# Optimization experiments

Hardware: AMD Instinct MI355X
Metric: run time of the kernel (lower is better)

## Reference

```python
import math
import jax, jax.numpy as jnp
import numpy as np
from jax import lax

N, C, H, W = 16, 128, 56, 56


def _conv(x, w, padding, dilation=(1, 1), groups=1):
    # NCHW conv matching torch.nn.Conv2d semantics (bias=False)
    return lax.conv_general_dilated(
        x, w, window_strides=(1, 1),
        padding=[(padding[0], padding[0]), (padding[1], padding[1])],
        rhs_dilation=dilation,
        dimension_numbers=('NCHW', 'OIHW', 'NCHW'),
        feature_group_count=groups)


def setup_inputs() -> dict:
    key = jax.random.key(0)
    ks = jax.random.split(key, 6)
    x = jax.random.normal(ks[0], (N, C, H, W), jnp.float32)
    w2 = jax.random.normal(ks[1], (C, C, 1, 3), jnp.float32) * 0.05   # dense 1x3 conv
    p6w = jax.random.normal(ks[2], (1, C, 7, 1), jnp.float32) * 0.02  # trunc_normal std=0.02
    w7 = jax.random.normal(ks[3], (C, 1, 1, 5), jnp.float32) * 0.05   # depthwise 1x5
    w8 = jax.random.normal(ks[4], (C, 1, 5, 5), jnp.float32) * 0.05   # depthwise 5x5 dil=2
    p9w = jax.random.normal(ks[5], (1, 1, 7, C), jnp.float32) * 0.02
    return {"x": x, "w2": w2, "p6w": p6w, "w7": w7, "w8": w8, "p9w": p9w}


def reference(x, w2, p6w, w7, w8, p9w):
    n, c, h, w = x.shape
    # t_1: F.unfold(x, (1,7), dilation=(1,2), padding=(0,6)) -> (n, c, 7, h, w)
    # tap k reads column j + 2k - 6 of x (zero padded)
    xp = jnp.pad(x, ((0, 0), (0, 0), (0, 0), (6, 6)))
    t1 = jnp.stack([xp[..., 2 * k:2 * k + w] for k in range(7)], axis=2)
    # t_2: dense (1,3) conv, padding (0,1)
    t2 = _conv(x, w2, (0, 1))
    # t_3: windowed channel correlation, (n, c, 7, c)
    t3 = jnp.einsum('nakhw,nbhw->nakb', t1, x) / math.sqrt(h * w)
    # t_4: F.unfold(t_2, (7,1), padding=(3,0)) -> (n, c, 7, h, w), taps along height
    t2p = jnp.pad(t2, ((0, 0), (0, 0), (3, 3), (0, 0)))
    t4 = jnp.stack([t2p[:, :, k:k + h, :] for k in range(7)], axis=2)
    # elementwise weighting
    t6 = p6w * t3          # (1,c,7,1) broadcast over (n,c,7,c)
    # depthwise convs
    t7 = _conv(t2, w7, (0, 2), groups=c)                 # (1,5) depthwise
    t8 = _conv(x, w8, (4, 4), dilation=(2, 2), groups=c)  # (5,5) depthwise, dil 2
    t9 = p9w * t6          # (1,1,7,c) broadcast
    # t_10: contract (c_in, tap) against windowed t4 -> (n, c, h, w)
    t10 = jnp.einsum('nakb,nakhw->nbhw', t9, t4) / math.sqrt(c * 7)
    t11 = t10 - t7
    t12 = t8 - t11
    return t12
```

## Files before the change

### kernel.cpp

```cpp
#include <hip/hip_runtime.h>

#define N_ 16
#define C_ 128
#define H_ 56
#define W_ 56
#define HW_ 3136

typedef __bf16 bf16x8 __attribute__((ext_vector_type(8)));
typedef __bf16 bf16x2 __attribute__((ext_vector_type(2)));
typedef float f32x4 __attribute__((ext_vector_type(4)));

#define XT_PER_N 401408
#define T2_PLANE 3472
#define T2_PER_N 444416
#define S_PER_N 114688
#define T10_PER_N 401408

#define WS_T10_OFF   3670016u
#define WS_T3_OFF    12845056u
#define WS_T2PB_OFF  20185088u
#define WS_W2B_OFF   34406400u

__global__ __launch_bounds__(256) void f0_prep(const float* __restrict__ x,
                                               const float* __restrict__ w2,
                                               __bf16* __restrict__ xT,
                                               __bf16* __restrict__ w2b,
                                               __bf16* __restrict__ t2pb) {
    int bid = blockIdx.x;
    int tid = threadIdx.x;
    if (bid < 2048) {
        int c = bid & 127, n = bid >> 7;
        __shared__ float xs[56 * 57];
        const float* xp = x + (size_t)(n * C_ + c) * HW_;
        for (int i = tid; i < HW_; i += 256) {
            int h = i / 56, w = i - 56 * h;
            xs[w * 57 + h] = xp[i];
        }
        __syncthreads();
        __bf16* op = xT + (size_t)(n * C_ + c) * HW_;
        for (int i = tid; i < 1568; i += 256) {
            int j = 2 * i;
            int wp = j / 56, h = j - 56 * wp;
            bf16x2 pr = {(__bf16)xs[wp * 57 + h], (__bf16)xs[wp * 57 + h + 1]};
            *(bf16x2*)&op[j] = pr;
        }
        __bf16* tp = t2pb + (size_t)(n * C_ + c) * T2_PLANE;
        for (int i = tid; i < 336; i += 256)
            tp[(i < 168) ? i : (3136 + i)] = (__bf16)0.f;
    } else {
        int idx = (bid - 2048) * 256 + tid;
        int co = idx / 384, kk = idx - co * 384;
        int j = kk >> 7, ci = kk & 127;
        w2b[idx] = (__bf16)w2[co * 384 + ci * 3 + j];
    }
}

__global__ __launch_bounds__(256) void f1_main(const float* __restrict__ x,
                                               const __bf16* __restrict__ w2b,
                                               const __bf16* __restrict__ xT,
                                               __bf16* __restrict__ t2pb,
                                               float* __restrict__ t3) {
    __shared__ __align__(16) char smem[36864];
    int bid = blockIdx.x;
    int tid = threadIdx.x;
    int wv = tid >> 6, lane = tid & 63;
    int lm = lane & 15, lq = lane >> 4;
    int wi = wv >> 1, wj = wv & 1;

    if (bid < 448) {
        int hc = bid & 3;
        int k = (bid >> 2) % 7;
        int n = bid / 28;
        int w_lo = 6 - 2 * k; if (w_lo < 0) w_lo = 0;
        int w_hi = 62 - 2 * k; if (w_hi > 56) w_hi = 56;
        int jlo = w_lo * 56;
        int L = (w_hi - w_lo) * 56;
        int T = (L + 63) >> 6;
        int shiftA = (2 * k - 6) * 56;

        __bf16* As = (__bf16*)smem;
        __bf16* Bs = (__bf16*)(smem + 18432);

        f32x4 acc[4][4];
        f32x4 zero4 = {0.f, 0.f, 0.f, 0.f};
#pragma unroll
        for (int i = 0; i < 4; i++)
#pragma unroll
            for (int j = 0; j < 4; j++) acc[i][j] = zero4;

        const __bf16* Ag = xT + (size_t)n * XT_PER_N + jlo + shiftA;
        const __bf16* Bg = xT + (size_t)n * XT_PER_N + jlo;
        __bf16 bz = (__bf16)0.f;
        bf16x8 vzero = {bz, bz, bz, bz, bz, bz, bz, bz};

        for (int c = hc; c < T; c += 4) {
            int off0 = c * 64;
#pragma unroll
            for (int u = 0; u < 4; u++) {
                int v = tid + u * 256;
                int m = v & 7, a = v >> 3;
                int jo = off0 + 8 * m;
                bool val = (jo + 8 <= L);
                bf16x8 va = val ? *(const bf16x8*)(Ag + (size_t)a * HW_ + jo) : vzero;
                bf16x8 vb = val ? *(const bf16x8*)(Bg + (size_t)a * HW_ + jo) : vzero;
                *(bf16x8*)&As[a * 72 + 8 * m] = va;
                *(bf16x8*)&Bs[a * 72 + 8 * m] = vb;
            }
            __syncthreads();
#pragma unroll
            for (int kb = 0; kb < 2; kb++) {
                bf16x8 av[4], bv[4];
#pragma unroll
                for (int i = 0; i < 4; i++)
                    av[i] = *(const bf16x8*)&As[(wi * 64 + i * 16 + lm) * 72 + kb * 32 + lq * 8];
#pragma unroll
                for (int j = 0; j < 4; j++)
                    bv[j] = *(const bf16x8*)&Bs[(wj * 64 + j * 16 + lm) * 72 + kb * 32 + lq * 8];
#pragma unroll
                for (int i = 0; i < 4; i++)
#pragma unroll
                    for (int j = 0; j < 4; j++)
                        acc[i][j] = __builtin_amdgcn_mfma_f32_16x16x32_bf16(av[i], bv[j], acc[i][j], 0, 0, 0);
            }
            __syncthreads();
        }

        float* t3p = t3 + (size_t)(n * 7 + k) * (C_ * C_);
        const float inv56 = 1.0f / 56.0f;
#pragma unroll
        for (int i = 0; i < 4; i++)
#pragma unroll
            for (int j = 0; j < 4; j++)
#pragma unroll
                for (int r = 0; r < 4; r++) {
                    int a = wi * 64 + i * 16 + lq * 4 + r;
                    int b = wj * 64 + j * 16 + lm;
                    atomicAdd(&t3p[a * C_ + b], acc[i][j][r] * inv56);
                }
    } else {
        int idx = bid - 448;
        int h = idx % 56, n = idx / 56;
        __bf16* Bs = (__bf16*)smem;
        float* kbuf = (float*)(smem + 17952);

        const float* xn = x + (size_t)n * C_ * HW_ + h * 56;
        for (int i = tid; i < 66 * 128; i += 256) {
            int ci = i / 66, wp = i - 66 * ci;
            int wx = wp - 1;
            float v = (wx >= 0 && wx < 56) ? xn[ci * HW_ + wx] : 0.f;
            Bs[wp * 136 + ci] = (__bf16)v;
        }

        f32x4 acc[4][2];
        f32x4 zero4 = {0.f, 0.f, 0.f, 0.f};
#pragma unroll
        for (int i = 0; i < 4; i++)
#pragma unroll
            for (int j = 0; j < 2; j++) acc[i][j] = zero4;

        __bf16* Asc = (__bf16*)(smem + 17952);
        __syncthreads();

        for (int c6 = 0; c6 < 6; c6++) {
#pragma unroll
            for (int u = 0; u < 4; u++) {
                int v = tid + u * 256;
                int m = v & 7, co = v >> 3;
                *(bf16x8*)&Asc[co * 72 + 8 * m] =
                    *(const bf16x8*)(w2b + co * 384 + c6 * 64 + 8 * m);
            }
            __syncthreads();
#pragma unroll
            for (int kl = 0; kl < 2; kl++) {
                int ks = c6 * 2 + kl;
                int j = ks >> 2;
                int cbase = (ks & 3) * 32;
                bf16x8 av[4], bv[2];
#pragma unroll
                for (int i = 0; i < 4; i++)
                    av[i] = *(const bf16x8*)&Asc[(wi * 64 + i * 16 + lm) * 72 + kl * 32 + lq * 8];
#pragma unroll
                for (int jt = 0; jt < 2; jt++) {
                    int row = wj * 32 + jt * 16 + lm + j;
                    bv[jt] = *(const bf16x8*)&Bs[row * 136 + cbase + lq * 8];
                }
#pragma unroll
                for (int i = 0; i < 4; i++)
#pragma unroll
                    for (int jt = 0; jt < 2; jt++)
                        acc[i][jt] = __builtin_amdgcn_mfma_f32_16x16x32_bf16(av[i], bv[jt], acc[i][jt], 0, 0, 0);
            }
            __syncthreads();
        }

        __bf16* t2n = t2pb + (size_t)n * T2_PER_N;
#pragma unroll 1
        for (int i = 0; i < 4; i++) {
            __syncthreads();
#pragma unroll
            for (int jt = 0; jt < 2; jt++)
#pragma unroll
                for (int r = 0; r < 4; r++)
                    kbuf[(wi * 16 + lq * 4 + r) * 65 + wj * 32 + jt * 16 + lm] = acc[i][jt][r];
            __syncthreads();
            int row = tid >> 3, seg = tid & 7;
            if (seg < 7) {
                int co = (row < 16) ? (i * 16 + row) : (64 + i * 16 + (row - 16));
                const float* src = &kbuf[row * 65 + seg * 8];
                bf16x8 o8;
#pragma unroll
                for (int d = 0; d < 8; d++) o8[d] = (__bf16)src[d];
                *(bf16x8*)(t2n + (size_t)co * T2_PLANE + (h + 3) * 56 + seg * 8) = o8;
            }
        }
    }
}

__global__ __launch_bounds__(256) void sprep(const float* __restrict__ t3,
                                             const float* __restrict__ p6w,
                                             const float* __restrict__ p9w,
                                             __bf16* __restrict__ s) {
    int idx = blockIdx.x * 256 + threadIdx.x;
    int n = idx / S_PER_N;
    int rem = idx - n * S_PER_N;
    int b = rem / 896;
    int ak = rem - b * 896;
    int a = ak / 7, k = ak - 7 * a;
    const float rs = 0.03340766f;
    float v = t3[((size_t)(n * 7 + k) * C_ + a) * C_ + b] * p6w[a * 7 + k] *
              p9w[k * C_ + b] * rs;
    s[idx] = (__bf16)v;
}

__global__ __launch_bounds__(256) void k3_mfma(const __bf16* __restrict__ s,
                                               const __bf16* __restrict__ t2pb,
                                               __bf16* __restrict__ t10) {
    int tile = blockIdx.x;
    int n = blockIdx.y;
    int hw0 = tile * 64;
    __shared__ __align__(16) __bf16 As[128 * 72];
    __shared__ __align__(16) __bf16 Bs[64 * 72];
    int tid = threadIdx.x;
    int wv = tid >> 6, lane = tid & 63;
    int lm = lane & 15, lq = lane >> 4;
    int wi = wv >> 1, wj = wv & 1;

    f32x4 acc[4][2];
    f32x4 zero4 = {0.f, 0.f, 0.f, 0.f};
#pragma unroll
    for (int i = 0; i < 4; i++)
#pragma unroll
        for (int j = 0; j < 2; j++) acc[i][j] = zero4;

    const __bf16* s_n = s + (size_t)n * S_PER_N;
    const __bf16* t2n = t2pb + (size_t)n * T2_PER_N;

    for (int kb = 0; kb < 14; kb++) {
#pragma unroll
        for (int u = 0; u < 4; u++) {
            int v = tid + u * 256;
            int m = v & 7, b = v >> 3;
            *(bf16x8*)&As[b * 72 + 8 * m] =
                *(const bf16x8*)(s_n + b * 896 + kb * 64 + 8 * m);
        }
        {
            int o = tid & 7;
            int p = tid >> 3;
            int ak0 = kb * 64 + 2 * p;
            int a0 = ak0 / 7, k0 = ak0 - 7 * a0;
            int ak1 = ak0 + 1;
            int a1 = ak1 / 7, k1 = ak1 - 7 * a1;
            int hwg = hw0 + 8 * o;
            bf16x8 v0 = *(const bf16x8*)(t2n + a0 * T2_PLANE + hwg + 56 * k0);
            bf16x8 v1 = *(const bf16x8*)(t2n + a1 * T2_PLANE + hwg + 56 * k1);
            int g = p >> 2;
            int off = (2 * p) & 7;
            int phys = ((g ^ o) << 3) + off;
#pragma unroll
            for (int j = 0; j < 8; j++) {
                int row = 8 * o + j;
                bf16x2 pr = {v0[j], v1[j]};
                *(bf16x2*)&Bs[row * 72 + phys] = pr;
            }
        }
        __syncthreads();
#pragma unroll
        for (int kbi = 0; kbi < 2; kbi++) {
            bf16x8 av[4], bv[2];
#pragma unroll
            for (int i = 0; i < 4; i++)
                av[i] = *(const bf16x8*)&As[(wi * 64 + i * 16 + lm) * 72 + kbi * 32 + lq * 8];
#pragma unroll
            for (int j = 0; j < 2; j++) {
                int row = wj * 32 + j * 16 + lm;
                int g = kbi * 4 + lq;
                int pg = g ^ (row >> 3);
                bv[j] = *(const bf16x8*)&Bs[row * 72 + pg * 8];
            }
#pragma unroll
            for (int i = 0; i < 4; i++)
#pragma unroll
                for (int j = 0; j < 2; j++)
                    acc[i][j] = __builtin_amdgcn_mfma_f32_16x16x32_bf16(av[i], bv[j], acc[i][j], 0, 0, 0);
        }
        __syncthreads();
    }

    float* buf = (float*)As;
    __bf16* t10n = t10 + (size_t)n * T10_PER_N;
#pragma unroll 1
    for (int i = 0; i < 4; i++) {
        __syncthreads();
#pragma unroll
        for (int j = 0; j < 2; j++)
#pragma unroll
            for (int r = 0; r < 4; r++)
                buf[(wi * 16 + lq * 4 + r) * 65 + wj * 32 + j * 16 + lm] = acc[i][j][r];
        __syncthreads();
        int row = tid >> 3, seg = tid & 7;
        int b = (row < 16) ? (i * 16 + row) : (64 + i * 16 + (row - 16));
        const float* src = &buf[row * 65 + seg * 8];
        bf16x8 o8;
#pragma unroll
        for (int d = 0; d < 8; d++) o8[d] = (__bf16)src[d];
        *(bf16x8*)(t10n + (size_t)b * HW_ + hw0 + seg * 8) = o8;
    }
}

__global__ __launch_bounds__(256) void d_final(const float* __restrict__ x,
                                               const __bf16* __restrict__ t2pb,
                                               const __bf16* __restrict__ t10,
                                               const float* __restrict__ w7,
                                               const float* __restrict__ w8,
                                               float* __restrict__ out) {
    int b = blockIdx.x, n = blockIdx.y;
    __shared__ float xs[64 * 65];
    __shared__ float t2s[56 * 60];
    int tid = threadIdx.x;
    const float* xp = x + (size_t)(n * C_ + b) * HW_;
    for (int i = tid; i < 64 * 65; i += 256) {
        int hh = i / 65, ww = i - 65 * hh;
        int h = hh - 4, w = ww - 4;
        float v = (h >= 0 && h < 56 && w >= 0 && w < 56) ? xp[h * 56 + w] : 0.f;
        xs[i] = v;
    }
    const __bf16* t2p = t2pb + (size_t)(n * C_ + b) * T2_PLANE;
    for (int i = tid; i < 56 * 60; i += 256) {
        int h = i / 60, ww = i - 60 * h;
        int w = ww - 2;
        float v = (w >= 0 && w < 56) ? (float)t2p[(h + 3) * 56 + w] : 0.f;
        t2s[i] = v;
    }
    __syncthreads();

    int r = tid >> 2;
    if (r >= 56) return;
    int w0 = (tid & 3) * 14;

    float w7r[5], w8r[25];
#pragma unroll
    for (int q = 0; q < 5; q++) w7r[q] = w7[b * 5 + q];
#pragma unroll
    for (int q = 0; q < 25; q++) w8r[q] = w8[b * 25 + q];

    float acc[14];
    {
        float tw[18];
#pragma unroll
        for (int c = 0; c < 18; c++) tw[c] = t2s[r * 60 + w0 + c];
#pragma unroll
        for (int i = 0; i < 14; i++)
            acc[i] = tw[i] * w7r[0] + tw[i + 1] * w7r[1] + tw[i + 2] * w7r[2] +
                     tw[i + 3] * w7r[3] + tw[i + 4] * w7r[4];
    }
#pragma unroll
    for (int p = 0; p < 5; p++) {
        float xv[22];
        int base = (r + 2 * p) * 65 + w0;
#pragma unroll
        for (int c = 0; c < 22; c++) xv[c] = xs[base + c];
#pragma unroll
        for (int i = 0; i < 14; i++)
            acc[i] += xv[i] * w8r[p * 5 + 0] + xv[i + 2] * w8r[p * 5 + 1] +
                      xv[i + 4] * w8r[p * 5 + 2] + xv[i + 6] * w8r[p * 5 + 3] +
                      xv[i + 8] * w8r[p * 5 + 4];
    }
    const __bf16* t10r = t10 + (size_t)(n * C_ + b) * HW_ + r * 56 + w0;
    float* outr = out + (size_t)(n * C_ + b) * HW_ + r * 56 + w0;
#pragma unroll
    for (int i = 0; i < 14; i++) outr[i] = acc[i] - (float)t10r[i];
}

extern "C" void kernel_launch(void* const* d_in, const int* in_sizes, int n_in,
                              void* d_out, int out_size, void* d_ws, size_t ws_size,
                              hipStream_t stream) {
    const float* x = (const float*)d_in[0];
    const float* w2 = (const float*)d_in[1];
    const float* p6w = (const float*)d_in[2];
    const float* w7 = (const float*)d_in[3];
    const float* w8 = (const float*)d_in[4];
    const float* p9w = (const float*)d_in[5];
    float* outp = (float*)d_out;

    char* ws = (char*)d_ws;
    __bf16* xT = (__bf16*)ws;
    __bf16* s = (__bf16*)ws;
    __bf16* t10 = (__bf16*)(ws + WS_T10_OFF);
    float* t3 = (float*)(ws + WS_T3_OFF);
    __bf16* t2pb = (__bf16*)(ws + WS_T2PB_OFF);
    __bf16* w2b = (__bf16*)(ws + WS_W2B_OFF);

    hipMemsetAsync(t3, 0, (size_t)N_ * 7 * C_ * C_ * sizeof(float), stream);

    f0_prep<<<dim3(2240), 256, 0, stream>>>(x, w2, xT, w2b, t2pb);
    f1_main<<<dim3(1344), 256, 0, stream>>>(x, w2b, xT, t2pb, t3);
    sprep<<<dim3((N_ * S_PER_N) / 256), 256, 0, stream>>>(t3, p6w, p9w, s);
    k3_mfma<<<dim3(49, N_), 256, 0, stream>>>(s, t2pb, t10);
    d_final<<<dim3(C_, N_), 256, 0, stream>>>(x, t2pb, t10, w7, w8, outp);
}
```

Before: 221.2 us.

## Exploit tap symmetry in channel correlation, prefetch global loads, fold memset into prep

The windowed channel correlation uses the fact that tap k and tap 6-k give transposed matrices, so only taps 0..3 are computed and sprep reads the transpose for taps 4..6. This cuts the correlation GEMM work by nearly half and shrinks the atomic-add output. The t3 zeroing moves from a separate memset into extra blocks of the prep kernel, removing one launch. All three MFMA loops now prefetch the next global tile into registers before the current compute, giving a register double-buffer that costs extra VGPRs.

Measured after the change: 210.2 us. 1.05x faster.

```diff
diff --git a/kernel.cpp b/kernel.cpp
--- a/kernel.cpp
+++ b/kernel.cpp
@@ -25,7 +25,8 @@
                                                const float* __restrict__ w2,
                                                __bf16* __restrict__ xT,
                                                __bf16* __restrict__ w2b,
-                                               __bf16* __restrict__ t2pb) {
+                                               __bf16* __restrict__ t2pb,
+                                               float* __restrict__ t3) {
     int bid = blockIdx.x;
     int tid = threadIdx.x;
     if (bid < 2048) {
@@ -47,11 +48,17 @@
         __bf16* tp = t2pb + (size_t)(n * C_ + c) * T2_PLANE;
         for (int i = tid; i < 336; i += 256)
             tp[(i < 168) ? i : (3136 + i)] = (__bf16)0.f;
-    } else {
+    } else if (bid < 2240) {
         int idx = (bid - 2048) * 256 + tid;
         int co = idx / 384, kk = idx - co * 384;
         int j = kk >> 7, ci = kk & 127;
         w2b[idx] = (__bf16)w2[co * 384 + ci * 3 + j];
+    } else {
+        f32x4 z4 = {0.f, 0.f, 0.f, 0.f};
+        f32x4* t4 = (f32x4*)t3;
+        int base = (bid - 2240) * 1024;
+#pragma unroll
+        for (int q = 0; q < 4; q++) t4[base + q * 256 + tid] = z4;
     }
 }
 
@@ -67,16 +74,13 @@
     int lm = lane & 15, lq = lane >> 4;
     int wi = wv >> 1, wj = wv & 1;
 
-    if (bid < 448) {
+    if (bid < 256) {
         int hc = bid & 3;
-        int k = (bid >> 2) % 7;
-        int n = bid / 28;
-        int w_lo = 6 - 2 * k; if (w_lo < 0) w_lo = 0;
-        int w_hi = 62 - 2 * k; if (w_hi > 56) w_hi = 56;
-        int jlo = w_lo * 56;
-        int L = (w_hi - w_lo) * 56;
+        int k = (bid >> 2) & 3;
+        int n = bid >> 4;
+        int w_lo = 6 - 2 * k;
+        int L = (56 - w_lo) * 56;
         int T = (L + 63) >> 6;
-        int shiftA = (2 * k - 6) * 56;
 
         __bf16* As = (__bf16*)smem;
         __bf16* Bs = (__bf16*)(smem + 18432);
@@ -88,25 +92,34 @@
 #pragma unroll
             for (int j = 0; j < 4; j++) acc[i][j] = zero4;
 
-        const __bf16* Ag = xT + (size_t)n * XT_PER_N + jlo + shiftA;
-        const __bf16* Bg = xT + (size_t)n * XT_PER_N + jlo;
+        const __bf16* Ag = xT + (size_t)n * XT_PER_N;
+        const __bf16* Bg = Ag + w_lo * 56;
         __bf16 bz = (__bf16)0.f;
         bf16x8 vzero = {bz, bz, bz, bz, bz, bz, bz, bz};
 
+        int m8 = tid & 7, abase = tid >> 3;
+        bf16x8 pva[4], pvb[4];
+        auto LOAD = [&](int c) {
+            int jo = c * 64 + 8 * m8;
+            bool val = (jo + 8 <= L);
+#pragma unroll
+            for (int u = 0; u < 4; u++) {
+                int a = abase + u * 32;
+                pva[u] = val ? *(const bf16x8*)(Ag + (size_t)a * HW_ + jo) : vzero;
+                pvb[u] = val ? *(const bf16x8*)(Bg + (size_t)a * HW_ + jo) : vzero;
+            }
+        };
+
+        LOAD(hc);
         for (int c = hc; c < T; c += 4) {
-            int off0 = c * 64;
 #pragma unroll
             for (int u = 0; u < 4; u++) {
-                int v = tid + u * 256;
-                int m = v & 7, a = v >> 3;
-                int jo = off0 + 8 * m;
-                bool val = (jo + 8 <= L);
-                bf16x8 va = val ? *(const bf16x8*)(Ag + (size_t)a * HW_ + jo) : vzero;
-                bf16x8 vb = val ? *(const bf16x8*)(Bg + (size_t)a * HW_ + jo) : vzero;
-                *(bf16x8*)&As[a * 72 + 8 * m] = va;
-                *(bf16x8*)&Bs[a * 72 + 8 * m] = vb;
-            }
-            __syncthreads();
+                int a = abase + u * 32;
+                *(bf16x8*)&As[a * 72 + 8 * m8] = pva[u];
+                *(bf16x8*)&Bs[a * 72 + 8 * m8] = pvb[u];
+            }
+            __syncthreads();
+            if (c + 4 < T) LOAD(c + 4);
 #pragma unroll
             for (int kb = 0; kb < 2; kb++) {
                 bf16x8 av[4], bv[4];
@@ -125,7 +138,7 @@
             __syncthreads();
         }
 
-        float* t3p = t3 + (size_t)(n * 7 + k) * (C_ * C_);
+        float* t3p = t3 + (size_t)(n * 4 + k) * (C_ * C_);
         const float inv56 = 1.0f / 56.0f;
 #pragma unroll
         for (int i = 0; i < 4; i++)
@@ -138,9 +151,10 @@
                     atomicAdd(&t3p[a * C_ + b], acc[i][j][r] * inv56);
                 }
     } else {
-        int idx = bid - 448;
+        int idx = bid - 256;
         int h = idx % 56, n = idx / 56;
         __bf16* Bs = (__bf16*)smem;
+        __bf16* Asc = (__bf16*)(smem + 17952);
         float* kbuf = (float*)(smem + 17952);
 
         const float* xn = x + (size_t)n * C_ * HW_ + h * 56;
@@ -158,18 +172,21 @@
 #pragma unroll
             for (int j = 0; j < 2; j++) acc[i][j] = zero4;
 
-        __bf16* Asc = (__bf16*)(smem + 17952);
-        __syncthreads();
-
+        int m8 = tid & 7, cobase = tid >> 3;
+        bf16x8 pA[4];
+        auto LOADA = [&](int c6) {
+#pragma unroll
+            for (int u = 0; u < 4; u++)
+                pA[u] = *(const bf16x8*)(w2b + (cobase + u * 32) * 384 + c6 * 64 + 8 * m8);
+        };
+
+        LOADA(0);
         for (int c6 = 0; c6 < 6; c6++) {
 #pragma unroll
-            for (int u = 0; u < 4; u++) {
-                int v = tid + u * 256;
-                int m = v & 7, co = v >> 3;
-                *(bf16x8*)&Asc[co * 72 + 8 * m] =
-                    *(const bf16x8*)(w2b + co * 384 + c6 * 64 + 8 * m);
-            }
-            __syncthreads();
+            for (int u = 0; u < 4; u++)
+                *(bf16x8*)&Asc[(cobase + u * 32) * 72 + 8 * m8] = pA[u];
+            __syncthreads();
+            if (c6 < 5) LOADA(c6 + 1);
 #pragma unroll
             for (int kl = 0; kl < 2; kl++) {
                 int ks = c6 * 2 + kl;
@@ -227,8 +244,10 @@
     int ak = rem - b * 896;
     int a = ak / 7, k = ak - 7 * a;
     const float rs = 0.03340766f;
-    float v = t3[((size_t)(n * 7 + k) * C_ + a) * C_ + b] * p6w[a * 7 + k] *
-              p9w[k * C_ + b] * rs;
+    float t3v = (k <= 3)
+                    ? t3[((size_t)(n * 4 + k) * C_ + a) * C_ + b]
+                    : t3[((size_t)(n * 4 + (6 - k)) * C_ + b) * C_ + a];
+    float v = t3v * p6w[a * 7 + k] * p9w[k * C_ + b] * rs;
     s[idx] = (__bf16)v;
 }
 
@@ -255,35 +274,42 @@
     const __bf16* s_n = s + (size_t)n * S_PER_N;
     const __bf16* t2n = t2pb + (size_t)n * T2_PER_N;
 
+    int m8 = tid & 7, bbase = tid >> 3;
+    int o = tid & 7;
+    int p = tid >> 3;
+    int g = p >> 2;
+    int off = (2 * p) & 7;
+    int phys = ((g ^ o) << 3) + off;
+
+    bf16x8 pS[4], pB0, pB1;
+    auto LOADC = [&](int kb) {
+#pragma unroll
+        for (int u = 0; u < 4; u++) {
+            int b = bbase + u * 32;
+            pS[u] = *(const bf16x8*)(s_n + b * 896 + kb * 64 + 8 * m8);
+        }
+        int ak0 = kb * 64 + 2 * p;
+        int a0 = ak0 / 7, k0 = ak0 - 7 * a0;
+        int ak1 = ak0 + 1;
+        int a1 = ak1 / 7, k1 = ak1 - 7 * a1;
+        int hwg = hw0 + 8 * o;
+        pB0 = *(const bf16x8*)(t2n + a0 * T2_PLANE + hwg + 56 * k0);
+        pB1 = *(const bf16x8*)(t2n + a1 * T2_PLANE + hwg + 56 * k1);
+    };
+
+    LOADC(0);
     for (int kb = 0; kb < 14; kb++) {
 #pragma unroll
-        for (int u = 0; u < 4; u++) {
-            int v = tid + u * 256;
-            int m = v & 7, b = v >> 3;
-            *(bf16x8*)&As[b * 72 + 8 * m] =
-                *(const bf16x8*)(s_n + b * 896 + kb * 64 + 8 * m);
-        }
-        {
-            int o = tid & 7;
-            int p = tid >> 3;
-            int ak0 = kb * 64 + 2 * p;
-            int a0 = ak0 / 7, k0 = ak0 - 7 * a0;
-            int ak1 = ak0 + 1;
-            int a1 = ak1 / 7, k1 = ak1 - 7 * a1;
-            int hwg = hw0 + 8 * o;
-            bf16x8 v0 = *(const bf16x8*)(t2n + a0 * T2_PLANE + hwg + 56 * k0);
-            bf16x8 v1 = *(const bf16x8*)(t2n + a1 * T2_PLANE + hwg + 56 * k1);
-            int g = p >> 2;
-            int off = (2 * p) & 7;
-            int phys = ((g ^ o) << 3) + off;
-#pragma unroll
-            for (int j = 0; j < 8; j++) {
-                int row = 8 * o + j;
-                bf16x2 pr = {v0[j], v1[j]};
-                *(bf16x2*)&Bs[row * 72 + phys] = pr;
-            }
+        for (int u = 0; u < 4; u++)
+            *(bf16x8*)&As[(bbase + u * 32) * 72 + 8 * m8] = pS[u];
+#pragma unroll
+        for (int j = 0; j < 8; j++) {
+            int row = 8 * o + j;
+            bf16x2 pr = {pB0[j], pB1[j]};
+            *(bf16x2*)&Bs[row * 72 + phys] = pr;
         }
         __syncthreads();
+        if (kb < 13) LOADC(kb + 1);
 #pragma unroll
         for (int kbi = 0; kbi < 2; kbi++) {
             bf16x8 av[4], bv[2];
@@ -293,8 +319,8 @@
 #pragma unroll
             for (int j = 0; j < 2; j++) {
                 int row = wj * 32 + j * 16 + lm;
-                int g = kbi * 4 + lq;
-                int pg = g ^ (row >> 3);
+                int gg = kbi * 4 + lq;
+                int pg = gg ^ (row >> 3);
                 bv[j] = *(const bf16x8*)&Bs[row * 72 + pg * 8];
             }
 #pragma unroll
@@ -410,10 +436,8 @@
     __bf16* t2pb = (__bf16*)(ws + WS_T2PB_OFF);
     __bf16* w2b = (__bf16*)(ws + WS_W2B_OFF);
 
-    hipMemsetAsync(t3, 0, (size_t)N_ * 7 * C_ * C_ * sizeof(float), stream);
-
-    f0_prep<<<dim3(2240), 256, 0, stream>>>(x, w2, xT, w2b, t2pb);
-    f1_main<<<dim3(1344), 256, 0, stream>>>(x, w2b, xT, t2pb, t3);
+    f0_prep<<<dim3(2496), 256, 0, stream>>>(x, w2, xT, w2b, t2pb, t3);
+    f1_main<<<dim3(1152), 256, 0, stream>>>(x, w2b, xT, t2pb, t3);
     sprep<<<dim3((N_ * S_PER_N) / 256), 256, 0, stream>>>(t3, p6w, p9w, s);
     k3_mfma<<<dim3(49, N_), 256, 0, stream>>>(s, t2pb, t10);
     d_final<<<dim3(C_, N_), 256, 0, stream>>>(x, t2pb, t10, w7, w8, outp);
```
